# Kernel optimization log

Measured on AMD Instinct MI355X. Metric: run time of the kernel, lower is better.

## Reference

```python
import jax, jax.numpy as jnp
import numpy as np

N = 100_000
E = 1_600_000
IN_DIM = 21
HID = 256
OUT = 256


def setup_inputs() -> dict:
    key = jax.random.key(0)
    ks = jax.random.split(key, 10)
    node_scalar = jax.random.normal(ks[0], (N, IN_DIM), dtype=jnp.float32)
    edge_index = jax.random.randint(ks[1], (2, E), 0, N, dtype=jnp.int64)
    s_in = 1.0 / np.sqrt(IN_DIM)
    s_h = 1.0 / np.sqrt(HID)
    W_in = jax.random.uniform(ks[2], (IN_DIM, HID), jnp.float32, -s_in, s_in)
    b_in = jax.random.uniform(ks[3], (HID,), jnp.float32, -s_in, s_in)
    W_self = jax.random.uniform(ks[4], (HID, HID), jnp.float32, -s_h, s_h)
    b_self = jax.random.uniform(ks[5], (HID,), jnp.float32, -s_h, s_h)
    W_nei = jax.random.uniform(ks[6], (HID, HID), jnp.float32, -s_h, s_h)
    b_nei = jax.random.uniform(ks[7], (HID,), jnp.float32, -s_h, s_h)
    W_out = jax.random.uniform(ks[8], (HID, OUT), jnp.float32, -s_h, s_h)
    b_out = jax.random.uniform(ks[9], (OUT,), jnp.float32, -s_h, s_h)
    return {
        "node_scalar": node_scalar,
        "W_in": W_in, "b_in": b_in,
        "W_self": W_self, "b_self": b_self,
        "W_nei": W_nei, "b_nei": b_nei,
        "W_out": W_out, "b_out": b_out,
        "edge_index": edge_index,
    }


def reference(node_scalar, W_in, b_in, W_self, b_self, W_nei, b_nei, W_out, b_out, edge_index):
    # x = relu(Linear(node_scalar)); dropout is identity in eval mode
    x = jax.nn.relu(node_scalar @ W_in + b_in)           # (N, H)
    n = x.shape[0]
    src, dst = edge_index[0], edge_index[1]
    msg = x[src]                                          # (E, H) gather
    agg = jax.ops.segment_sum(msg, dst, num_segments=n)   # (N, H) scatter-add
    deg = jax.ops.segment_sum(jnp.ones((dst.shape[0],), dtype=x.dtype), dst, num_segments=n)
    agg = agg / jnp.maximum(deg, 1.0)[:, None]            # degree mean (clamp_min 1)
    h = jax.nn.relu(x @ W_self + b_self + agg @ W_nei + b_nei)
    g = h.mean(axis=0)                                    # global mean pool -> (H,)
    return g @ W_out + b_out                              # (OUT,)
```

## Files before the change

kernel.cpp:

```cpp
#include <hip/hip_runtime.h>
#include <hip/hip_bf16.h>

#define HID 256
#define IND 21
#define ASTR 40
#define PB 3200
#define MAXB 512

typedef short short8 __attribute__((ext_vector_type(8)));
typedef float floatx4 __attribute__((ext_vector_type(4)));
typedef float floatx2 __attribute__((ext_vector_type(2)));

__device__ inline unsigned short f2bf(float f) {
  __hip_bfloat16 h = __float2bfloat16(f);
  union { __hip_bfloat16 h; unsigned short u; } c;
  c.h = h;
  return c.u;
}

__device__ inline unsigned int pk_bf16_trunc(floatx2 p) {
  union { float f; unsigned int u; } a, b;
  a.f = p.x; b.f = p.y;
  return (b.u & 0xffff0000u) | (a.u >> 16);
}

__device__ inline void acc8p(uint2 v, floatx2* a) {
  a[0] += __builtin_amdgcn_cvt_pk_f32_fp8((int)v.x, false);
  a[1] += __builtin_amdgcn_cvt_pk_f32_fp8((int)v.x, true);
  a[2] += __builtin_amdgcn_cvt_pk_f32_fp8((int)v.y, false);
  a[3] += __builtin_amdgcn_cvt_pk_f32_fp8((int)v.y, true);
}

__global__ __launch_bounds__(256) void k_front(
    const float* __restrict__ ns, const float* __restrict__ Win,
    const float* __restrict__ bin, unsigned int* __restrict__ xq,
    const float* __restrict__ Wself, const float* __restrict__ Wnei,
    unsigned short* __restrict__ WcT,
    const int* __restrict__ dst, int* __restrict__ bcnt,
    int N, int E, int nb2, int G1) {
  int blk = blockIdx.x;
  int tid = threadIdx.x;
  if (blk < G1) {
    __shared__ float s[8][IND];
    __shared__ float fx[8][257];
    int nb = blk * 8;
    if (tid < 8 * IND) {
      int idx = nb * IND + tid;
      s[tid / IND][tid % IND] = (idx < N * IND) ? ns[idx] : 0.f;
    }
    float w[IND];
#pragma unroll
    for (int k = 0; k < IND; k++) w[k] = Win[k * HID + tid];
    float b = bin[tid];
    __syncthreads();
#pragma unroll
    for (int j = 0; j < 8; j++) {
      float acc = b;
#pragma unroll
      for (int k = 0; k < IND; k++) acc += s[j][k] * w[k];
      fx[j][tid] = acc > 0.f ? acc : 0.f;
    }
    __syncthreads();
#pragma unroll
    for (int t = 0; t < 2; t++) {
      int wi = tid + t * 256;
      int j = wi >> 6, cw = wi & 63;
      int node = nb + j;
      if (node < N) {
        const float* fp = &fx[j][cw * 4];
        int lo = __builtin_amdgcn_cvt_pk_fp8_f32(fp[0], fp[1], 0, false);
        int full = __builtin_amdgcn_cvt_pk_fp8_f32(fp[2], fp[3], lo, true);
        xq[(size_t)node * 64 + cw] = (unsigned int)full;
      }
    }
  } else if (blk < G1 + 256) {
    int n = blk - G1;
#pragma unroll
    for (int t = 0; t < 2; t++) {
      int k = tid + t * 256;
      float v = (k < HID) ? Wself[k * HID + n] : Wnei[(k - HID) * HID + n];
      WcT[n * 512 + k] = f2bf(v);
    }
  } else {
    __shared__ int lh[MAXB];
    int e0 = (blk - G1 - 256) * PB;
    for (int b = tid; b < nb2; b += 256) lh[b] = 0;
    __syncthreads();
    int c = min(PB, E - e0);
    for (int i = tid; i < c; i += 256) atomicAdd(&lh[dst[e0 + i] >> 8], 1);
    __syncthreads();
    for (int b = tid; b < nb2; b += 256)
      if (lh[b]) atomicAdd(&bcnt[b], lh[b]);
  }
}

__global__ __launch_bounds__(512) void k_bscan(
    const int* __restrict__ bcnt, int* __restrict__ bbase, int* __restrict__ bcur,
    int* __restrict__ row_start, int E, int N, int nb2) {
  __shared__ int ts[512];
  int tid = threadIdx.x;
  int v = (tid < nb2) ? bcnt[tid] : 0;
  ts[tid] = v;
  __syncthreads();
  for (int off = 1; off < 512; off <<= 1) {
    int t = (tid >= off) ? ts[tid - off] : 0;
    __syncthreads();
    ts[tid] += t;
    __syncthreads();
  }
  if (tid < nb2) { bbase[tid] = ts[tid] - v; bcur[tid] = ts[tid] - v; }
  if (tid == 0) { bbase[nb2] = E; row_start[N] = E; }
}

__global__ __launch_bounds__(256) void k_part(
    const int* __restrict__ src, const int* __restrict__ dst,
    int* __restrict__ bcur, uint2* __restrict__ ebuf, int E, int nb2) {
  __shared__ int lh[MAXB];
  int tid = threadIdx.x;
  int e0 = blockIdx.x * PB;
  for (int b = tid; b < nb2; b += 256) lh[b] = 0;
  __syncthreads();
  int cnt = min(PB, E - e0);
  for (int i = tid; i < cnt; i += 256) atomicAdd(&lh[dst[e0 + i] >> 8], 1);
  __syncthreads();
  for (int b = tid; b < nb2; b += 256) {
    int c = lh[b];
    lh[b] = (c > 0) ? atomicAdd(&bcur[b], c) : 0;
  }
  __syncthreads();
  for (int i = tid; i < cnt; i += 256) {
    int s = src[e0 + i];
    int d = dst[e0 + i];
    int pos = atomicAdd(&lh[d >> 8], 1);
    ebuf[pos] = make_uint2((unsigned)s, (unsigned)d);
  }
}

__global__ __launch_bounds__(256) void k_fill2(
    const uint2* __restrict__ ebuf, const int* __restrict__ bbase,
    int* __restrict__ row_start, int* __restrict__ csr, int N) {
  __shared__ int lcnt[256];
  __shared__ int lcur[256];
  __shared__ int ts[256];
  int b = blockIdx.x;
  int tid = threadIdx.x;
  int start = bbase[b], end = bbase[b + 1];
  lcnt[tid] = 0;
  __syncthreads();
  for (int i = start + tid; i < end; i += 256)
    atomicAdd(&lcnt[ebuf[i].y & 255], 1);
  __syncthreads();
  int v = lcnt[tid];
  ts[tid] = v;
  __syncthreads();
  for (int off = 1; off < 256; off <<= 1) {
    int t = (tid >= off) ? ts[tid - off] : 0;
    __syncthreads();
    ts[tid] += t;
    __syncthreads();
  }
  int excl = start + ts[tid] - v;
  int node = (b << 8) + tid;
  if (node < N) row_start[node] = excl;
  lcur[tid] = excl;
  __syncthreads();
  for (int i = start + tid; i < end; i += 256) {
    uint2 e = ebuf[i];
    int pos = atomicAdd(&lcur[e.y & 255], 1);
    csr[pos] = (int)e.x;
  }
}

__global__ __launch_bounds__(256) void k_agg(
    const uint2* __restrict__ xq, const int* __restrict__ csr,
    const int* __restrict__ row_start, uint2* __restrict__ aggq, int N) {
  int wid = (int)((blockIdx.x * (unsigned)blockDim.x + threadIdx.x) >> 6);
  int lane = threadIdx.x & 63;
  int half = lane >> 5;
  int l32 = lane & 31;
  if (wid >= N) return;
  int start = row_start[wid];
  int end = row_start[wid + 1];
  int c = end - start;
  floatx2 a[4], b[4], d[4], e[4];
#pragma unroll
  for (int j = 0; j < 4; j++) {
    a[j] = (floatx2){0.f, 0.f}; b[j] = (floatx2){0.f, 0.f};
    d[j] = (floatx2){0.f, 0.f}; e[j] = (floatx2){0.f, 0.f};
  }

  int i = 0;
  for (; i + 8 <= c; i += 8) {
    int s0 = csr[start + i + half];
    int s1 = csr[start + i + 2 + half];
    int s2 = csr[start + i + 4 + half];
    int s3 = csr[start + i + 6 + half];
    uint2 v0 = xq[(size_t)s0 * 32 + l32];
    uint2 v1 = xq[(size_t)s1 * 32 + l32];
    uint2 v2 = xq[(size_t)s2 * 32 + l32];
    uint2 v3 = xq[(size_t)s3 * 32 + l32];
    acc8p(v0, a); acc8p(v1, b); acc8p(v2, d); acc8p(v3, e);
  }
  for (; i + 2 <= c; i += 2) {
    int s0 = csr[start + i + half];
    uint2 v0 = xq[(size_t)s0 * 32 + l32];
    acc8p(v0, a);
  }
  if ((c & 1) && half == 0) {
    int s0 = csr[start + c - 1];
    uint2 v0 = xq[(size_t)s0 * 32 + l32];
    acc8p(v0, a);
  }
#pragma unroll
  for (int j = 0; j < 4; j++) a[j] += b[j] + d[j] + e[j];

  float f[8];
#pragma unroll
  for (int j = 0; j < 4; j++) { f[2 * j] = a[j].x; f[2 * j + 1] = a[j].y; }
#pragma unroll
  for (int j = 0; j < 8; j++) f[j] += __shfl_xor(f[j], 32);

  if (half == 0) {
    float inv = 1.0f / fmaxf((float)c, 1.0f);
#pragma unroll
    for (int j = 0; j < 8; j++) f[j] *= inv;
    int lo0 = __builtin_amdgcn_cvt_pk_fp8_f32(f[0], f[1], 0, false);
    int w0  = __builtin_amdgcn_cvt_pk_fp8_f32(f[2], f[3], lo0, true);
    int lo1 = __builtin_amdgcn_cvt_pk_fp8_f32(f[4], f[5], 0, false);
    int w1  = __builtin_amdgcn_cvt_pk_fp8_f32(f[6], f[7], lo1, true);
    aggq[(size_t)wid * 32 + l32] = make_uint2((unsigned)w0, (unsigned)w1);
  }
}

__global__ __launch_bounds__(256, 2) void k_h(
    const unsigned char* __restrict__ xq8, const unsigned char* __restrict__ aggq8,
    const unsigned short* __restrict__ WcT, const float* __restrict__ bself,
    const float* __restrict__ bnei, float* __restrict__ gsum, int N) {
  __shared__ __align__(16) unsigned short As[128 * ASTR];
  __shared__ __align__(16) unsigned short Bs[256 * ASTR];
  __shared__ float colsum[256];
  int tid = threadIdx.x;
  int rowBase = blockIdx.x * 128;
  int lane = tid & 63;
  int wid = tid >> 6;
  int wr = wid >> 1, wc = wid & 1;
  int n16 = lane & 15, quad = lane >> 4;

  colsum[tid] = 0.f;

  floatx4 acc[4][8];
#pragma unroll
  for (int i = 0; i < 4; i++)
#pragma unroll
    for (int j = 0; j < 8; j++) acc[i][j] = (floatx4){0.f, 0.f, 0.f, 0.f};

  int ar = tid >> 1;
  int as = tid & 1;
  int gr = rowBase + ar;
  if (gr >= N) gr = N - 1;

  for (int k0 = 0; k0 < 512; k0 += 32) {
    const unsigned char* abase = (k0 < HID) ? xq8 : aggq8;
    int kc = k0 & 255;
    uint4 v = *(const uint4*)(abase + (size_t)gr * HID + kc + as * 16);
    unsigned int w[8];
    {
      unsigned int src4[4] = {v.x, v.y, v.z, v.w};
#pragma unroll
      for (int j = 0; j < 4; j++) {
        floatx2 p0 = __builtin_amdgcn_cvt_pk_f32_fp8((int)src4[j], false);
        floatx2 p1 = __builtin_amdgcn_cvt_pk_f32_fp8((int)src4[j], true);
        w[2 * j] = pk_bf16_trunc(p0);
        w[2 * j + 1] = pk_bf16_trunc(p1);
      }
    }
    *(uint4*)(&As[ar * ASTR + as * 16]) = make_uint4(w[0], w[1], w[2], w[3]);
    *(uint4*)(&As[ar * ASTR + as * 16 + 8]) = make_uint4(w[4], w[5], w[6], w[7]);
#pragma unroll
    for (int j = 0; j < 4; j++) {
      int idx = tid + j * 256;
      int r = idx >> 2;
      int s = idx & 3;
      uint4 vb = *(const uint4*)(WcT + (size_t)r * 512 + k0 + s * 8);
      *(uint4*)(&Bs[r * ASTR + s * 8]) = vb;
    }
    __syncthreads();

    short8 af[4];
#pragma unroll
    for (int rt = 0; rt < 4; rt++)
      af[rt] = *(const short8*)&As[(wr * 64 + rt * 16 + n16) * ASTR + quad * 8];
#pragma unroll
    for (int ct = 0; ct < 8; ct++) {
      short8 bf = *(const short8*)&Bs[(wc * 128 + ct * 16 + n16) * ASTR + quad * 8];
#pragma unroll
      for (int rt = 0; rt < 4; rt++)
        acc[rt][ct] = __builtin_amdgcn_mfma_f32_16x16x32_bf16(
            af[rt], bf, acc[rt][ct], 0, 0, 0);
    }
    __syncthreads();
  }

#pragma unroll
  for (int ct = 0; ct < 8; ct++) {
    int gcol = wc * 128 + ct * 16 + n16;
    float bb = bself[gcol] + bnei[gcol];
    float psum = 0.f;
#pragma unroll
    for (int rt = 0; rt < 4; rt++) {
#pragma unroll
      for (int r = 0; r < 4; r++) {
        int row = rowBase + wr * 64 + rt * 16 + quad * 4 + r;
        float v = acc[rt][ct][r] + bb;
        v = v > 0.f ? v : 0.f;
        if (row < N) psum += v;
      }
    }
    atomicAdd(&colsum[gcol], psum);
  }
  __syncthreads();
  atomicAdd(&gsum[tid], colsum[tid]);
}

__global__ __launch_bounds__(HID) void k_out(
    const float* __restrict__ gsum, const float* __restrict__ Wout,
    const float* __restrict__ bout, float* __restrict__ out, float invN) {
  __shared__ float g[HID];
  int c = threadIdx.x;
  g[c] = gsum[c] * invN;
  __syncthreads();
  float acc = bout[c];
#pragma unroll 8
  for (int k = 0; k < HID; k++) acc += g[k] * Wout[k * HID + c];
  out[c] = acc;
}

extern "C" void kernel_launch(void* const* d_in, const int* in_sizes, int n_in,
                              void* d_out, int out_size, void* d_ws, size_t ws_size,
                              hipStream_t stream) {
  const float* ns    = (const float*)d_in[0];
  const float* Win   = (const float*)d_in[1];
  const float* bin   = (const float*)d_in[2];
  const float* Wself = (const float*)d_in[3];
  const float* bself = (const float*)d_in[4];
  const float* Wnei  = (const float*)d_in[5];
  const float* bnei  = (const float*)d_in[6];
  const float* Wout  = (const float*)d_in[7];
  const float* bout  = (const float*)d_in[8];
  const int*   eidx  = (const int*)d_in[9];

  int N = in_sizes[0] / IND;
  int E = in_sizes[9] / 2;
  const int* src = eidx;
  const int* dst = eidx + E;
  int nb2 = (N + 255) >> 8;

  unsigned int* xq    = (unsigned int*)d_ws;
  unsigned int* aggq  = xq + (size_t)N * 64;
  unsigned short* WcT = (unsigned short*)(aggq + (size_t)N * 64);
  int* csr       = (int*)(WcT + 256 * 512);
  uint2* ebuf    = (uint2*)(csr + E);
  int* row_start = (int*)(ebuf + E);
  int* bcnt      = row_start + N + 1;
  int* bbase     = bcnt + MAXB;
  int* bcur      = bbase + MAXB + 1;
  float* gsum    = (float*)(bcur + MAXB);

  hipMemsetAsync(bcnt, 0, MAXB * sizeof(int), stream);
  hipMemsetAsync(gsum, 0, HID * sizeof(float), stream);

  int G1 = (N + 7) / 8;
  int pgrid = (E + PB - 1) / PB;
  k_front<<<G1 + 256 + pgrid, 256, 0, stream>>>(
      ns, Win, bin, xq, Wself, Wnei, WcT, dst, bcnt, N, E, nb2, G1);

  k_bscan<<<1, 512, 0, stream>>>(bcnt, bbase, bcur, row_start, E, N, nb2);
  k_part<<<pgrid, 256, 0, stream>>>(src, dst, bcur, ebuf, E, nb2);
  k_fill2<<<nb2, 256, 0, stream>>>(ebuf, bbase, row_start, csr, N);

  int agrid = (N + 3) / 4;
  k_agg<<<agrid, 256, 0, stream>>>((const uint2*)xq, csr, row_start,
                                   (uint2*)aggq, N);

  int hgrid = (N + 127) / 128;
  k_h<<<hgrid, 256, 0, stream>>>((const unsigned char*)xq,
                                 (const unsigned char*)aggq,
                                 WcT, bself, bnei, gsum, N);

  k_out<<<1, HID, 0, stream>>>(gsum, Wout, bout, (float*)d_out, 1.0f / (float)N);
}
```

Baseline: 322.0 us.

## Rewrite GEMM to LDS-free 32x32 MFMA with prepacked weights, pack edge buffer

```diff
diff --git a/kernel.cpp b/kernel.cpp
--- a/kernel.cpp
+++ b/kernel.cpp
@@ -3,12 +3,11 @@
 
 #define HID 256
 #define IND 21
-#define ASTR 40
-#define PB 3200
+#define PB 6400
 #define MAXB 512
 
 typedef short short8 __attribute__((ext_vector_type(8)));
-typedef float floatx4 __attribute__((ext_vector_type(4)));
+typedef float floatx16 __attribute__((ext_vector_type(16)));
 typedef float floatx2 __attribute__((ext_vector_type(2)));
 
 __device__ inline unsigned short f2bf(float f) {
@@ -31,11 +30,26 @@
   a[3] += __builtin_amdgcn_cvt_pk_f32_fp8((int)v.y, true);
 }
 
+__device__ inline short8 mk_s8(unsigned a, unsigned b, unsigned c, unsigned d) {
+  union { uint4 u; short8 s; } x; x.u = make_uint4(a, b, c, d); return x.s;
+}
+__device__ inline short8 u4_s8(uint4 v) {
+  union { uint4 u; short8 s; } x; x.u = v; return x.s;
+}
+
+__device__ inline short8 dec8(uint2 v) {
+  unsigned w0 = pk_bf16_trunc(__builtin_amdgcn_cvt_pk_f32_fp8((int)v.x, false));
+  unsigned w1 = pk_bf16_trunc(__builtin_amdgcn_cvt_pk_f32_fp8((int)v.x, true));
+  unsigned w2 = pk_bf16_trunc(__builtin_amdgcn_cvt_pk_f32_fp8((int)v.y, false));
+  unsigned w3 = pk_bf16_trunc(__builtin_amdgcn_cvt_pk_f32_fp8((int)v.y, true));
+  return mk_s8(w0, w1, w2, w3);
+}
+
 __global__ __launch_bounds__(256) void k_front(
     const float* __restrict__ ns, const float* __restrict__ Win,
     const float* __restrict__ bin, unsigned int* __restrict__ xq,
     const float* __restrict__ Wself, const float* __restrict__ Wnei,
-    unsigned short* __restrict__ WcT,
+    unsigned short* __restrict__ Bf16,
     const int* __restrict__ dst, int* __restrict__ bcnt,
     int N, int E, int nb2, int G1) {
   int blk = blockIdx.x;
@@ -75,11 +89,15 @@
     }
   } else if (blk < G1 + 256) {
     int n = blk - G1;
+    int ct = n >> 5, l5 = n & 31;
 #pragma unroll
     for (int t = 0; t < 2; t++) {
       int k = tid + t * 256;
       float v = (k < HID) ? Wself[k * HID + n] : Wnei[(k - HID) * HID + n];
-      WcT[n * 512 + k] = f2bf(v);
+      int c = k >> 4, kin = k & 15;
+      int lane = (kin >> 3) * 32 + l5;
+      int j = kin & 7;
+      Bf16[(size_t)((c * 8 + ct) * 64 + lane) * 8 + j] = f2bf(v);
     }
   } else {
     __shared__ int lh[MAXB];
@@ -114,7 +132,7 @@
 
 __global__ __launch_bounds__(256) void k_part(
     const int* __restrict__ src, const int* __restrict__ dst,
-    int* __restrict__ bcur, uint2* __restrict__ ebuf, int E, int nb2) {
+    int* __restrict__ bcur, unsigned int* __restrict__ ebuf, int E, int nb2) {
   __shared__ int lh[MAXB];
   int tid = threadIdx.x;
   int e0 = blockIdx.x * PB;
@@ -132,12 +150,12 @@
     int s = src[e0 + i];
     int d = dst[e0 + i];
     int pos = atomicAdd(&lh[d >> 8], 1);
-    ebuf[pos] = make_uint2((unsigned)s, (unsigned)d);
+    ebuf[pos] = ((unsigned)s << 8) | ((unsigned)d & 255u);
   }
 }
 
 __global__ __launch_bounds__(256) void k_fill2(
-    const uint2* __restrict__ ebuf, const int* __restrict__ bbase,
+    const unsigned int* __restrict__ ebuf, const int* __restrict__ bbase,
     int* __restrict__ row_start, int* __restrict__ csr, int N) {
   __shared__ int lcnt[256];
   __shared__ int lcur[256];
@@ -148,7 +166,7 @@
   lcnt[tid] = 0;
   __syncthreads();
   for (int i = start + tid; i < end; i += 256)
-    atomicAdd(&lcnt[ebuf[i].y & 255], 1);
+    atomicAdd(&lcnt[ebuf[i] & 255u], 1);
   __syncthreads();
   int v = lcnt[tid];
   ts[tid] = v;
@@ -165,9 +183,9 @@
   lcur[tid] = excl;
   __syncthreads();
   for (int i = start + tid; i < end; i += 256) {
-    uint2 e = ebuf[i];
-    int pos = atomicAdd(&lcur[e.y & 255], 1);
-    csr[pos] = (int)e.x;
+    unsigned int e = ebuf[i];
+    int pos = atomicAdd(&lcur[e & 255u], 1);
+    csr[pos] = (int)(e >> 8);
   }
 }
 
@@ -188,7 +206,6 @@
     a[j] = (floatx2){0.f, 0.f}; b[j] = (floatx2){0.f, 0.f};
     d[j] = (floatx2){0.f, 0.f}; e[j] = (floatx2){0.f, 0.f};
   }
-
   int i = 0;
   for (; i + 8 <= c; i += 8) {
     int s0 = csr[start + i + half];
@@ -234,89 +251,52 @@
 
 __global__ __launch_bounds__(256, 2) void k_h(
     const unsigned char* __restrict__ xq8, const unsigned char* __restrict__ aggq8,
-    const unsigned short* __restrict__ WcT, const float* __restrict__ bself,
+    const uint4* __restrict__ Bf, const float* __restrict__ bself,
     const float* __restrict__ bnei, float* __restrict__ gsum, int N) {
-  __shared__ __align__(16) unsigned short As[128 * ASTR];
-  __shared__ __align__(16) unsigned short Bs[256 * ASTR];
   __shared__ float colsum[256];
   int tid = threadIdx.x;
-  int rowBase = blockIdx.x * 128;
   int lane = tid & 63;
-  int wid = tid >> 6;
-  int wr = wid >> 1, wc = wid & 1;
-  int n16 = lane & 15, quad = lane >> 4;
+  int w = tid >> 6;
+  int l32 = lane & 31;
+  int half = lane >> 5;
+  int rowBase = blockIdx.x * 128 + w * 32;
+  int row = rowBase + l32;
+  if (row >= N) row = N - 1;
 
   colsum[tid] = 0.f;
-
-  floatx4 acc[4][8];
-#pragma unroll
-  for (int i = 0; i < 4; i++)
-#pragma unroll
-    for (int j = 0; j < 8; j++) acc[i][j] = (floatx4){0.f, 0.f, 0.f, 0.f};
-
-  int ar = tid >> 1;
-  int as = tid & 1;
-  int gr = rowBase + ar;
-  if (gr >= N) gr = N - 1;
-
-  for (int k0 = 0; k0 < 512; k0 += 32) {
-    const unsigned char* abase = (k0 < HID) ? xq8 : aggq8;
-    int kc = k0 & 255;
-    uint4 v = *(const uint4*)(abase + (size_t)gr * HID + kc + as * 16);
-    unsigned int w[8];
-    {
-      unsigned int src4[4] = {v.x, v.y, v.z, v.w};
-#pragma unroll
-      for (int j = 0; j < 4; j++) {
-        floatx2 p0 = __builtin_amdgcn_cvt_pk_f32_fp8((int)src4[j], false);
-        floatx2 p1 = __builtin_amdgcn_cvt_pk_f32_fp8((int)src4[j], true);
-        w[2 * j] = pk_bf16_trunc(p0);
-        w[2 * j + 1] = pk_bf16_trunc(p1);
-      }
-    }
-    *(uint4*)(&As[ar * ASTR + as * 16]) = make_uint4(w[0], w[1], w[2], w[3]);
-    *(uint4*)(&As[ar * ASTR + as * 16 + 8]) = make_uint4(w[4], w[5], w[6], w[7]);
-#pragma unroll
-    for (int j = 0; j < 4; j++) {
-      int idx = tid + j * 256;
-      int r = idx >> 2;
-      int s = idx & 3;
-      uint4 vb = *(const uint4*)(WcT + (size_t)r * 512 + k0 + s * 8);
-      *(uint4*)(&Bs[r * ASTR + s * 8]) = vb;
-    }
-    __syncthreads();
-
-    short8 af[4];
-#pragma unroll
-    for (int rt = 0; rt < 4; rt++)
-      af[rt] = *(const short8*)&As[(wr * 64 + rt * 16 + n16) * ASTR + quad * 8];
+  __syncthreads();
+
+  floatx16 acc[8];
+#pragma unroll
+  for (int j = 0; j < 8; j++) acc[j] = (floatx16)(0.f);
+
+  size_t aoff = (size_t)row * HID + half * 8;
+
+  for (int c = 0; c < 32; c++) {
+    const unsigned char* ab = (c < 16) ? xq8 : aggq8;
+    uint2 va = *(const uint2*)(ab + aoff + (size_t)(c & 15) * 16);
+    short8 af = dec8(va);
+    const uint4* bp = Bf + (size_t)c * 512 + lane;
 #pragma unroll
     for (int ct = 0; ct < 8; ct++) {
-      short8 bf = *(const short8*)&Bs[(wc * 128 + ct * 16 + n16) * ASTR + quad * 8];
-#pragma unroll
-      for (int rt = 0; rt < 4; rt++)
-        acc[rt][ct] = __builtin_amdgcn_mfma_f32_16x16x32_bf16(
-            af[rt], bf, acc[rt][ct], 0, 0, 0);
-    }
-    __syncthreads();
+      short8 bf = u4_s8(bp[ct * 64]);
+      acc[ct] = __builtin_amdgcn_mfma_f32_32x32x16_bf16(af, bf, acc[ct], 0, 0, 0);
+    }
   }
 
 #pragma unroll
   for (int ct = 0; ct < 8; ct++) {
-    int gcol = wc * 128 + ct * 16 + n16;
-    float bb = bself[gcol] + bnei[gcol];
+    int col = ct * 32 + l32;
+    float bb = bself[col] + bnei[col];
     float psum = 0.f;
 #pragma unroll
-    for (int rt = 0; rt < 4; rt++) {
-#pragma unroll
-      for (int r = 0; r < 4; r++) {
-        int row = rowBase + wr * 64 + rt * 16 + quad * 4 + r;
-        float v = acc[rt][ct][r] + bb;
-        v = v > 0.f ? v : 0.f;
-        if (row < N) psum += v;
-      }
-    }
-    atomicAdd(&colsum[gcol], psum);
+    for (int r = 0; r < 16; r++) {
+      int rw = rowBase + (r & 3) + 8 * (r >> 2) + 4 * half;
+      float v = acc[ct][r] + bb;
+      v = v > 0.f ? v : 0.f;
+      if (rw < N) psum += v;
+    }
+    atomicAdd(&colsum[col], psum);
   }
   __syncthreads();
   atomicAdd(&gsum[tid], colsum[tid]);
@@ -357,9 +337,9 @@
 
   unsigned int* xq    = (unsigned int*)d_ws;
   unsigned int* aggq  = xq + (size_t)N * 64;
-  unsigned short* WcT = (unsigned short*)(aggq + (size_t)N * 64);
-  int* csr       = (int*)(WcT + 256 * 512);
-  uint2* ebuf    = (uint2*)(csr + E);
+  unsigned short* Bf16 = (unsigned short*)(aggq + (size_t)N * 64);
+  int* csr       = (int*)(Bf16 + 256 * 512);
+  unsigned int* ebuf = (unsigned int*)(csr + E);
   int* row_start = (int*)(ebuf + E);
   int* bcnt      = row_start + N + 1;
   int* bbase     = bcnt + MAXB;
@@ -372,7 +352,7 @@
   int G1 = (N + 7) / 8;
   int pgrid = (E + PB - 1) / PB;
   k_front<<<G1 + 256 + pgrid, 256, 0, stream>>>(
-      ns, Win, bin, xq, Wself, Wnei, WcT, dst, bcnt, N, E, nb2, G1);
+      ns, Win, bin, xq, Wself, Wnei, Bf16, dst, bcnt, N, E, nb2, G1);
 
   k_bscan<<<1, 512, 0, stream>>>(bcnt, bbase, bcur, row_start, E, N, nb2);
   k_part<<<pgrid, 256, 0, stream>>>(src, dst, bcur, ebuf, E, nb2);
@@ -385,7 +365,7 @@
   int hgrid = (N + 127) / 128;
   k_h<<<hgrid, 256, 0, stream>>>((const unsigned char*)xq,
                                  (const unsigned char*)aggq,
-                                 WcT, bself, bnei, gsum, N);
+                                 (const uint4*)Bf16, bself, bnei, gsum, N);
 
   k_out<<<1, HID, 0, stream>>>(gsum, Wout, bout, (float*)d_out, 1.0f / (float)N);
 }
```

After: 345.3 us. 1.07x slower.
